# Performance work log

Measured on AMD Instinct MI355X. Metric: run time of the kernel, lower is better.

The kernel has to match this reference:

```python
import jax, jax.numpy as jnp
import numpy as np

# ---- Cl(3,0) Cayley table; blade order [1, e1,e2,e3, e12,e13,e23, e123] ----
def _build_cayley():
    blades = [0b000, 0b001, 0b010, 0b100, 0b011, 0b101, 0b110, 0b111]
    pos = {b: i for i, b in enumerate(blades)}
    def sign(a, b):
        s, a = 0, a >> 1
        while a:
            s += bin(a & b).count('1')
            a >>= 1
        return -1.0 if s & 1 else 1.0
    C = np.zeros((8, 8, 8), np.float32)
    for i, a in enumerate(blades):
        for k, b in enumerate(blades):
            C[i, pos[a ^ b], k] = sign(a, b)  # e_a * e_b -> sign * e_(a^b), metric all +1
    return jnp.asarray(C)

CAYLEY = _build_cayley()
EPS = 1e-6
SEQ = 25      # num_nodes (5) + num_edges (20)
HEADS = 8

def _expand_grades(w):
    # [..., 4] (per-grade) -> [..., 8] (per-blade), grade dims 1,3,3,1
    return jnp.concatenate([w[..., 0:1],
                            jnp.repeat(w[..., 1:2], 3, -1),
                            jnp.repeat(w[..., 2:3], 3, -1),
                            w[..., 3:4]], axis=-1)

def mv_linear(x, w, b):
    # x [N, in, 8], w [out, in, 4], b [out]; bias only on scalar blade
    y = jnp.einsum('nmi,omi->noi', x, _expand_grades(w))
    return y.at[..., 0].add(b)

def mv_layernorm(x, a):
    n = jnp.linalg.norm(x, axis=-1, keepdims=True)   # [N, c, 1] multivector norm
    n = jnp.mean(n, axis=1, keepdims=True) + EPS     # mean over channels -> [N, 1, 1]
    return a[None, :, None] * x / n

def mv_silu(x, a, b):
    # invariants: scalar component + squared grade magnitudes (mag2)
    inv = jnp.stack([x[..., 0],
                     jnp.sum(x[..., 1:4] ** 2, -1),
                     jnp.sum(x[..., 4:7] ** 2, -1),
                     x[..., 7] ** 2], axis=-1)       # [N, c, 4]
    return _expand_grades(jax.nn.sigmoid(a * inv + b)) * x

def geometric_product(a, b):
    return jnp.einsum('nci,ijk,nck->ncj', a, CAYLEY, b)


def setup_inputs() -> dict:
    key = jax.random.key(0)
    ks = iter(jax.random.split(key, 40))
    D, B = 128, 1024
    N = B * SEQ
    s = 0.05
    rn = lambda *sh: jax.random.normal(next(ks), sh, jnp.float32) * s
    return dict(
        src=jax.random.normal(next(ks), (N, D, 8), jnp.float32),
        ln1_a=jnp.ones(D, jnp.float32), ln2_a=jnp.ones(D, jnp.float32), ln3_a=jnp.ones(D, jnp.float32),
        wq=rn(D, D, 4), bq=jnp.zeros(D, jnp.float32),
        wk=rn(D, D, 4), bk=jnp.zeros(D, jnp.float32),
        wv=rn(D, D, 4), bv=jnp.zeros(D, jnp.float32),
        wo=rn(D, D, 4), bo=jnp.zeros(D, jnp.float32),
        gw1=rn(2 * D, D, 4), gb1=jnp.zeros(2 * D, jnp.float32),
        gw2=rn(2 * D, D, 4), gb2=jnp.zeros(2 * D, jnp.float32),
        gw3=rn(D, 2 * D, 4), gb3=jnp.zeros(D, jnp.float32),
        gna=jnp.ones(D, jnp.float32),
        mw1=rn(2 * D, D, 4), mb1=jnp.zeros(2 * D, jnp.float32),
        sa=jnp.ones((2 * D, 4), jnp.float32), sb=jnp.zeros((2 * D, 4), jnp.float32),
        mw2=rn(D, 2 * D, 4), mb2=jnp.zeros(D, jnp.float32),
    )


def reference(src, ln1_a, ln2_a, ln3_a, wq, bq, wk, bk, wv, bv, wo, bo,
              gw1, gb1, gw2, gb2, gw3, gb3, gna,
              mw1, mb1, sa, sb, mw2, mb2):
    N, D, _ = src.shape
    B, dh = N // SEQ, D // HEADS

    def attention(x):
        q = mv_linear(x, wq, bq).reshape(B, SEQ, HEADS, dh, 8)
        k = mv_linear(x, wk, bk).reshape(B, SEQ, HEADS, dh, 8)
        v = mv_linear(x, wv, bv).reshape(B, SEQ, HEADS, dh, 8)
        scores = jnp.einsum('bshdi,bthdi->bhst', q, k) / np.float32(np.sqrt(dh * 8))
        p = jax.nn.softmax(scores, axis=-1)
        o = jnp.einsum('bhst,bthdi->bshdi', p, v).reshape(N, D, 8)
        return mv_linear(o, wo, bo)

    # pre-norm attention + residual
    x = src + attention(mv_layernorm(src, ln1_a))
    x = mv_layernorm(x, ln2_a)
    # GP_Layer: two grade-wise linears -> geometric product -> linear -> norm
    xl = mv_linear(x, gw1, gb1)
    xr = mv_linear(x, gw2, gb2)
    g = mv_layernorm(mv_linear(geometric_product(xl, xr), gw3, gb3), gna)
    x = x + g
    x = mv_layernorm(x, ln3_a)
    # gated MLP: MVLinear -> MVSiLU -> MVLinear
    ff = mv_linear(mv_silu(mv_linear(x, mw1, mb1), sa, sb), mw2, mb2)
    return x + ff
```

## Files before the change

### kernel.cpp

```cpp
#include <hip/hip_runtime.h>
#include <hip/hip_bf16.h>
#include <math.h>

#define NROWS 25600
#define SEQL  25
#define EPSV  1e-6f

typedef __hip_bfloat16 bf16;
typedef __attribute__((ext_vector_type(4))) float f32x4;
typedef __attribute__((ext_vector_type(8))) short bf16x8;
typedef unsigned int u32;

#define GLD16(gp_, lp_) __builtin_amdgcn_global_load_lds( \
    (const __attribute__((address_space(1))) u32*)(gp_), \
    (__attribute__((address_space(3))) u32*)(lp_), 16, 0, 0)

__device__ __forceinline__ void gprod(const float* a, const float* b, float* r) {
  const int M[8] = {0,1,2,4,3,5,6,7};
  const int P[8] = {0,1,2,4,3,5,6,7};
#pragma unroll
  for (int i = 0; i < 8; ++i) {
    const int ma = M[i];
#pragma unroll
    for (int k = 0; k < 8; ++k) {
      const int mb = M[k];
      int par = 0;
      for (int t = ma >> 1; t; t >>= 1) par += __popc(t & mb);
      const float s = (par & 1) ? -1.f : 1.f;
      r[P[ma ^ mb]] += s * a[i] * b[k];
    }
  }
}

template<int KT, int ON>
__global__ __launch_bounds__(256) void gemm_kernel(
    const bf16* __restrict__ A, const bf16* __restrict__ W,
    const float* __restrict__ bias, const float* __restrict__ invnm,
    bf16* __restrict__ Y)
{
  __shared__ __align__(16) short As[128 * 128];
  __shared__ __align__(16) short Bs[128 * 128];
  const int tid  = threadIdx.x;
  const int lane = tid & 63;
  const int wid  = tid >> 6;
  const int pl   = blockIdx.z;
  const int g    = (pl == 0) ? 0 : ((pl < 4) ? 1 : ((pl < 7) ? 2 : 3));
  const size_t n0 = (size_t)blockIdx.x * 128;
  const int c0    = blockIdx.y * 128;
  const bf16* Ab = A + (size_t)pl * NROWS * KT + n0 * KT;
  const bf16* Wb = W + ((size_t)g * ON + c0) * KT;

  f32x4 acc[4][4];
#pragma unroll
  for (int i = 0; i < 4; ++i)
#pragma unroll
    for (int j = 0; j < 4; ++j) acc[i][j] = (f32x4){0.f, 0.f, 0.f, 0.f};

  const int wm = (wid & 1) * 64;
  const int wn = (wid >> 1) * 64;
  const int srow = wid * 32 + (lane >> 4);
  const int scol = (lane & 15) * 8;

  constexpr int NC = KT / 128;
#pragma unroll
  for (int kc = 0; kc < NC; ++kc) {
#pragma unroll
    for (int j = 0; j < 8; ++j) {
      const bf16* ga = Ab + (size_t)(srow + j * 4) * KT + kc * 128 + scol;
      const bf16* gb = Wb + (size_t)(srow + j * 4) * KT + kc * 128 + scol;
      GLD16(ga, &As[wid * 4096 + j * 512]);
      GLD16(gb, &Bs[wid * 4096 + j * 512]);
    }
    __syncthreads();
#pragma unroll
    for (int ks = 0; ks < 4; ++ks) {
      bf16x8 af[4], bg[4];
#pragma unroll
      for (int i = 0; i < 4; ++i) {
        af[i] = *(const bf16x8*)&As[(wm + i * 16 + (lane & 15)) * 128 + ks * 32 + (lane >> 4) * 8];
        bg[i] = *(const bf16x8*)&Bs[(wn + i * 16 + (lane & 15)) * 128 + ks * 32 + (lane >> 4) * 8];
      }
#pragma unroll
      for (int mi = 0; mi < 4; ++mi)
#pragma unroll
        for (int ni = 0; ni < 4; ++ni)
          acc[mi][ni] = __builtin_amdgcn_mfma_f32_16x16x32_bf16(af[mi], bg[ni], acc[mi][ni], 0, 0, 0);
    }
    if (kc + 1 < NC) __syncthreads();
  }

  const int cr = (lane >> 4) * 4;
  const int cc = lane & 15;
  bf16* Yb = Y + (size_t)pl * NROWS * ON;
#pragma unroll
  for (int mi = 0; mi < 4; ++mi) {
#pragma unroll
    for (int j = 0; j < 4; ++j) {
      const size_t n = n0 + wm + mi * 16 + cr + j;
      const float sc = invnm ? invnm[n] : 1.f;
#pragma unroll
      for (int ni = 0; ni < 4; ++ni) {
        const int colg = c0 + wn + ni * 16 + cc;
        float v = acc[mi][ni][j] * sc;
        if (pl == 0) v += bias[colg];
        Yb[n * ON + colg] = __float2bfloat16(v);
      }
    }
  }
}

__global__ __launch_bounds__(256) void wprep_kernel(
    const float* __restrict__ w, const float* __restrict__ lnscale,
    bf16* __restrict__ out, int O, int K)
{
  const int idx = blockIdx.x * 256 + threadIdx.x;
  if (idx >= O * K) return;
  const int k = idx % K;
  const float s = lnscale ? lnscale[k] : 1.f;
  const float4 wv = *(const float4*)(w + (size_t)idx * 4);
  const size_t P = (size_t)O * K;
  out[0 * P + idx] = __float2bfloat16(wv.x * s);
  out[1 * P + idx] = __float2bfloat16(wv.y * s);
  out[2 * P + idx] = __float2bfloat16(wv.z * s);
  out[3 * P + idx] = __float2bfloat16(wv.w * s);
}

__global__ __launch_bounds__(256) void repack_kernel(
    const float* __restrict__ src, bf16* __restrict__ Xp, float* __restrict__ nminv)
{
  __shared__ float red[256];
  const int tid = threadIdx.x;
  const size_t n = (size_t)blockIdx.x * 2 + (tid >> 7);
  const int c = tid & 127;
  const size_t P = (size_t)NROWS * 128;
  const size_t idx = n * 128 + c;
  const float* sp = src + idx * 8;
  float v[8];
  const float4 s0 = *(const float4*)sp;
  const float4 s1 = *(const float4*)(sp + 4);
  v[0]=s0.x; v[1]=s0.y; v[2]=s0.z; v[3]=s0.w;
  v[4]=s1.x; v[5]=s1.y; v[6]=s1.z; v[7]=s1.w;
  float ss = 0.f;
#pragma unroll
  for (int p = 0; p < 8; ++p) {
    Xp[p * P + idx] = __float2bfloat16(v[p]);
    ss += v[p] * v[p];
  }
  red[tid] = sqrtf(ss);
  __syncthreads();
  for (int off = 64; off > 0; off >>= 1) {
    if ((tid & 127) < off) red[tid] += red[tid + off];
    __syncthreads();
  }
  if (c == 0) nminv[n] = 1.f / (red[tid] / 128.f + EPSV);
}

__global__ __launch_bounds__(256) void attn_kernel(
    bf16* __restrict__ Q, const bf16* __restrict__ K, const bf16* __restrict__ V)
{
  __shared__ float Pld[4][32 * 36];
  const int tid  = threadIdx.x;
  const int lane = tid & 63;
  const int wid  = tid >> 6;
  const int job  = blockIdx.x * 4 + wid;
  const int b    = job >> 3;
  const int h    = job & 7;
  const size_t PS = (size_t)NROWS * 128;
  const int rowbase = b * SEQL;
  const int l15 = lane & 15;
  const int lg  = lane >> 4;

  f32x4 acc[2][2];
#pragma unroll
  for (int si = 0; si < 2; ++si)
#pragma unroll
    for (int ti = 0; ti < 2; ++ti) acc[si][ti] = (f32x4){0.f,0.f,0.f,0.f};

#pragma unroll
  for (int ks = 0; ks < 4; ++ks) {
    const int f = ks * 32 + lg * 8;
    const int p = f >> 4, d = f & 15;
    bf16x8 aq[2], bk[2];
#pragma unroll
    for (int si = 0; si < 2; ++si) {
      int s = si * 16 + l15; if (s > 24) s = 24;
      aq[si] = *(const bf16x8*)(Q + (size_t)p * PS + (size_t)(rowbase + s) * 128 + h * 16 + d);
    }
#pragma unroll
    for (int ti = 0; ti < 2; ++ti) {
      int t = ti * 16 + l15; if (t > 24) t = 24;
      bk[ti] = *(const bf16x8*)(K + (size_t)p * PS + (size_t)(rowbase + t) * 128 + h * 16 + d);
    }
#pragma unroll
    for (int si = 0; si < 2; ++si)
#pragma unroll
      for (int ti = 0; ti < 2; ++ti)
        acc[si][ti] = __builtin_amdgcn_mfma_f32_16x16x32_bf16(aq[si], bk[ti], acc[si][ti], 0, 0, 0);
  }

  const float scale = 0.08838834764831845f;
  float pv[2][2][4];
#pragma unroll
  for (int si = 0; si < 2; ++si)
#pragma unroll
    for (int ti = 0; ti < 2; ++ti)
#pragma unroll
      for (int r = 0; r < 4; ++r) {
        float v = acc[si][ti][r] * scale;
        if (ti * 16 + l15 > 24) v = -1e30f;
        pv[si][ti][r] = v;
      }
#pragma unroll
  for (int si = 0; si < 2; ++si)
#pragma unroll
    for (int r = 0; r < 4; ++r) {
      float m = fmaxf(pv[si][0][r], pv[si][1][r]);
#pragma unroll
      for (int off = 1; off < 16; off <<= 1) m = fmaxf(m, __shfl_xor(m, off));
      const float e0 = __expf(pv[si][0][r] - m);
      const float e1 = __expf(pv[si][1][r] - m);
      float sum = e0 + e1;
#pragma unroll
      for (int off = 1; off < 16; off <<= 1) sum += __shfl_xor(sum, off);
      const float inv = 1.f / sum;
      pv[si][0][r] = e0 * inv;
      pv[si][1][r] = e1 * inv;
    }

  float* Pw = &Pld[wid][0];
#pragma unroll
  for (int si = 0; si < 2; ++si)
#pragma unroll
    for (int ti = 0; ti < 2; ++ti)
#pragma unroll
      for (int r = 0; r < 4; ++r)
        Pw[(si * 16 + lg * 4 + r) * 36 + ti * 16 + l15] = pv[si][ti][r];
  __syncthreads();

  const int p2 = lane >> 3;
  const int d2 = (lane & 7) * 2;
  const bf16* vb = V + (size_t)p2 * PS + (size_t)rowbase * 128 + h * 16 + d2;
  float vlo[32], vhi[32];
#pragma unroll
  for (int t = 0; t < SEQL; ++t) {
    const __hip_bfloat162 vv = *(const __hip_bfloat162*)(vb + (size_t)t * 128);
    vlo[t] = __bfloat162float(vv.x);
    vhi[t] = __bfloat162float(vv.y);
  }
#pragma unroll
  for (int t = SEQL; t < 32; ++t) { vlo[t] = 0.f; vhi[t] = 0.f; }

  bf16* ob = Q + (size_t)p2 * PS + (size_t)rowbase * 128 + h * 16 + d2;
  for (int s = 0; s < SEQL; ++s) {
    const float4* pr = reinterpret_cast<const float4*>(&Pld[wid][s * 36]);
    float a0 = 0.f, a1 = 0.f;
#pragma unroll
    for (int t4 = 0; t4 < 8; ++t4) {
      const float4 pq = pr[t4];
      a0 += pq.x * vlo[t4*4+0] + pq.y * vlo[t4*4+1] + pq.z * vlo[t4*4+2] + pq.w * vlo[t4*4+3];
      a1 += pq.x * vhi[t4*4+0] + pq.y * vhi[t4*4+1] + pq.z * vhi[t4*4+2] + pq.w * vhi[t4*4+3];
    }
    __hip_bfloat162 o2;
    o2.x = __float2bfloat16(a0);
    o2.y = __float2bfloat16(a1);
    *(__hip_bfloat162*)(ob + (size_t)s * 128) = o2;
  }
}

__global__ __launch_bounds__(256) void xres_kernel(
    const float* __restrict__ src, const bf16* __restrict__ AO,
    bf16* __restrict__ X, float* __restrict__ nminv)
{
  __shared__ float red[256];
  const int tid = threadIdx.x;
  const size_t n = (size_t)blockIdx.x * 2 + (tid >> 7);
  const int c = tid & 127;
  const size_t P = (size_t)NROWS * 128;
  const size_t idx = n * 128 + c;
  const float* sp = src + idx * 8;
  float v[8];
  const float4 s0 = *(const float4*)sp;
  const float4 s1 = *(const float4*)(sp + 4);
  v[0]=s0.x; v[1]=s0.y; v[2]=s0.z; v[3]=s0.w;
  v[4]=s1.x; v[5]=s1.y; v[6]=s1.z; v[7]=s1.w;
  float ss = 0.f;
#pragma unroll
  for (int p = 0; p < 8; ++p) {
    v[p] += __bfloat162float(AO[p * P + idx]);
    X[p * P + idx] = __float2bfloat16(v[p]);
    ss += v[p] * v[p];
  }
  red[tid] = sqrtf(ss);
  __syncthreads();
  for (int off = 64; off > 0; off >>= 1) {
    if ((tid & 127) < off) red[tid] += red[tid + off];
    __syncthreads();
  }
  if (c == 0) nminv[n] = 1.f / (red[tid] / 128.f + EPSV);
}

__global__ __launch_bounds__(256) void gp_kernel(
    bf16* __restrict__ XL, const bf16* __restrict__ XR)
{
  const size_t idx = (size_t)blockIdx.x * 256 + threadIdx.x;
  const size_t P = (size_t)NROWS * 256;
  float a[8], b[8], r[8] = {0.f,0.f,0.f,0.f,0.f,0.f,0.f,0.f};
#pragma unroll
  for (int p = 0; p < 8; ++p) {
    a[p] = __bfloat162float(XL[p * P + idx]);
    b[p] = __bfloat162float(XR[p * P + idx]);
  }
  gprod(a, b, r);
#pragma unroll
  for (int p = 0; p < 8; ++p) XL[p * P + idx] = __float2bfloat16(r[p]);
}

__global__ __launch_bounds__(256) void combine_kernel(
    bf16* __restrict__ X, const bf16* __restrict__ Gl,
    const float* __restrict__ ln2a, const float* __restrict__ gna,
    const float* __restrict__ nm2inv, float* __restrict__ nm4inv)
{
  __shared__ float red[256];
  const int tid = threadIdx.x;
  const size_t n = (size_t)blockIdx.x * 2 + (tid >> 7);
  const int c = tid & 127;
  const size_t P = (size_t)NROWS * 128;
  const size_t idx = n * 128 + c;

  float gv[8];
  float ssg = 0.f;
#pragma unroll
  for (int p = 0; p < 8; ++p) {
    gv[p] = __bfloat162float(Gl[p * P + idx]);
    ssg += gv[p] * gv[p];
  }
  red[tid] = sqrtf(ssg);
  __syncthreads();
  for (int off = 64; off > 0; off >>= 1) {
    if ((tid & 127) < off) red[tid] += red[tid + off];
    __syncthreads();
  }
  const float invg = 1.f / (red[tid & 128] / 128.f + EPSV);
  __syncthreads();

  const float s2 = ln2a[c] * nm2inv[n];
  const float sg = gna[c] * invg;
  float ss = 0.f;
#pragma unroll
  for (int p = 0; p < 8; ++p) {
    const float v = s2 * __bfloat162float(X[p * P + idx]) + sg * gv[p];
    X[p * P + idx] = __float2bfloat16(v);
    ss += v * v;
  }
  red[tid] = sqrtf(ss);
  __syncthreads();
  for (int off = 64; off > 0; off >>= 1) {
    if ((tid & 127) < off) red[tid] += red[tid + off];
    __syncthreads();
  }
  if (c == 0) nm4inv[n] = 1.f / (red[tid] / 128.f + EPSV);
}

__global__ __launch_bounds__(256) void silu_kernel(
    bf16* __restrict__ H, const float* __restrict__ sa, const float* __restrict__ sb)
{
  const size_t idx = (size_t)blockIdx.x * 256 + threadIdx.x;
  const int c = (int)(idx & 255);
  const size_t P = (size_t)NROWS * 256;
  float v[8];
#pragma unroll
  for (int p = 0; p < 8; ++p) v[p] = __bfloat162float(H[p * P + idx]);
  const float i0 = v[0];
  const float i1 = v[1]*v[1] + v[2]*v[2] + v[3]*v[3];
  const float i2 = v[4]*v[4] + v[5]*v[5] + v[6]*v[6];
  const float i3 = v[7]*v[7];
  const float g0 = 1.f / (1.f + expf(-(sa[c*4+0]*i0 + sb[c*4+0])));
  const float g1 = 1.f / (1.f + expf(-(sa[c*4+1]*i1 + sb[c*4+1])));
  const float g2 = 1.f / (1.f + expf(-(sa[c*4+2]*i2 + sb[c*4+2])));
  const float g3 = 1.f / (1.f + expf(-(sa[c*4+3]*i3 + sb[c*4+3])));
  v[0]*=g0; v[1]*=g1; v[2]*=g1; v[3]*=g1; v[4]*=g2; v[5]*=g2; v[6]*=g2; v[7]*=g3;
#pragma unroll
  for (int p = 0; p < 8; ++p) H[p * P + idx] = __float2bfloat16(v[p]);
}

__global__ __launch_bounds__(256) void final_kernel(
    const bf16* __restrict__ X3, const bf16* __restrict__ FF,
    const float* __restrict__ ln3a, const float* __restrict__ nm4inv,
    float* __restrict__ out)
{
  const size_t idx = (size_t)blockIdx.x * 256 + threadIdx.x;
  const int c = (int)(idx & 127);
  const size_t n = idx >> 7;
  const size_t P = (size_t)NROWS * 128;
  const float s = ln3a[c] * nm4inv[n];
  float o[8];
#pragma unroll
  for (int p = 0; p < 8; ++p)
    o[p] = s * __bfloat162float(X3[p * P + idx]) + __bfloat162float(FF[p * P + idx]);
  float4 lo, hi;
  lo.x=o[0]; lo.y=o[1]; lo.z=o[2]; lo.w=o[3];
  hi.x=o[4]; hi.y=o[5]; hi.z=o[6]; hi.w=o[7];
  *reinterpret_cast<float4*>(out + idx * 8)     = lo;
  *reinterpret_cast<float4*>(out + idx * 8 + 4) = hi;
}

extern "C" void kernel_launch(void* const* d_in, const int* in_sizes, int n_in,
                              void* d_out, int out_size, void* d_ws, size_t ws_size,
                              hipStream_t stream) {
  (void)in_sizes; (void)n_in; (void)out_size; (void)ws_size;
  const float* src   = (const float*)d_in[0];
  const float* ln1_a = (const float*)d_in[1];
  const float* ln2_a = (const float*)d_in[2];
  const float* ln3_a = (const float*)d_in[3];
  const float* wq = (const float*)d_in[4];  const float* bq = (const float*)d_in[5];
  const float* wk = (const float*)d_in[6];  const float* bk = (const float*)d_in[7];
  const float* wv = (const float*)d_in[8];  const float* bv = (const float*)d_in[9];
  const float* wo = (const float*)d_in[10]; const float* bo = (const float*)d_in[11];
  const float* gw1 = (const float*)d_in[12]; const float* gb1 = (const float*)d_in[13];
  const float* gw2 = (const float*)d_in[14]; const float* gb2 = (const float*)d_in[15];
  const float* gw3 = (const float*)d_in[16]; const float* gb3 = (const float*)d_in[17];
  const float* gna = (const float*)d_in[18];
  const float* mw1 = (const float*)d_in[19]; const float* mb1 = (const float*)d_in[20];
  const float* sa  = (const float*)d_in[21]; const float* sb  = (const float*)d_in[22];
  const float* mw2 = (const float*)d_in[23]; const float* mb2 = (const float*)d_in[24];

  const size_t P128 = (size_t)NROWS * 128;
  char* ws = (char*)d_ws;
  bf16* R1 = (bf16*)ws;
  bf16* R2 = (bf16*)(ws + 104857600);
  bf16* WQ = (bf16*)(ws + 157286400);
  bf16* WK = WQ + 65536;
  bf16* WV = WK + 65536;
  bf16* WO = WV + 65536;
  bf16* WG1 = WO + 65536;
  bf16* WG2 = WG1 + 131072;
  bf16* WG3 = WG2 + 131072;
  bf16* WM1 = WG3 + 131072;
  bf16* WM2 = WM1 + 131072;
  float* nm1 = (float*)(ws + 159121408);
  float* nm2 = nm1 + NROWS;
  float* nm4 = nm2 + NROWS;

  bf16* Dd = (bf16*)d_out;
  bf16* Xp = R2;
  bf16* Kp = R1;
  bf16* Vp = R1 + P128;

  wprep_kernel<<<64, 256, 0, stream>>>(wq, ln1_a, WQ, 128, 128);
  wprep_kernel<<<64, 256, 0, stream>>>(wk, ln1_a, WK, 128, 128);
  wprep_kernel<<<64, 256, 0, stream>>>(wv, ln1_a, WV, 128, 128);
  wprep_kernel<<<64, 256, 0, stream>>>(wo, nullptr, WO, 128, 128);
  wprep_kernel<<<128, 256, 0, stream>>>(gw1, ln2_a, WG1, 256, 128);
  wprep_kernel<<<128, 256, 0, stream>>>(gw2, ln2_a, WG2, 256, 128);
  wprep_kernel<<<128, 256, 0, stream>>>(gw3, nullptr, WG3, 128, 256);
  wprep_kernel<<<128, 256, 0, stream>>>(mw1, ln3_a, WM1, 256, 128);
  wprep_kernel<<<128, 256, 0, stream>>>(mw2, nullptr, WM2, 128, 256);

  repack_kernel<<<NROWS / 2, 256, 0, stream>>>(src, Xp, nm1);

  dim3 g128(NROWS / 128, 1, 8), g256(NROWS / 128, 2, 8);
  gemm_kernel<128, 128><<<g128, 256, 0, stream>>>(Xp, WQ, bq, nm1, Dd);
  gemm_kernel<128, 128><<<g128, 256, 0, stream>>>(Xp, WK, bk, nm1, Kp);
  gemm_kernel<128, 128><<<g128, 256, 0, stream>>>(Xp, WV, bv, nm1, Vp);

  attn_kernel<<<2048, 256, 0, stream>>>(Dd, Kp, Vp);

  gemm_kernel<128, 128><<<g128, 256, 0, stream>>>(Dd, WO, bo, nullptr, Kp);

  xres_kernel<<<NROWS / 2, 256, 0, stream>>>(src, Kp, Xp, nm2);

  gemm_kernel<128, 256><<<g256, 256, 0, stream>>>(Xp, WG1, gb1, nm2, Dd);
  gemm_kernel<128, 256><<<g256, 256, 0, stream>>>(Xp, WG2, gb2, nm2, R1);

  gp_kernel<<<NROWS, 256, 0, stream>>>(Dd, R1);

  gemm_kernel<256, 128><<<g128, 256, 0, stream>>>(Dd, WG3, gb3, nullptr, Kp);

  combine_kernel<<<NROWS / 2, 256, 0, stream>>>(Xp, Kp, ln2_a, gna, nm2, nm4);

  gemm_kernel<128, 256><<<g256, 256, 0, stream>>>(Xp, WM1, mb1, nm4, Dd);

  silu_kernel<<<NROWS, 256, 0, stream>>>(Dd, sa, sb);

  gemm_kernel<256, 128><<<g128, 256, 0, stream>>>(Dd, WM2, mb2, nullptr, Vp);

  final_kernel<<<(NROWS * 128) / 256, 256, 0, stream>>>(Xp, Vp, ln3_a, nm4, (float*)d_out);
}
```

Before: 681.2 us.

## Swizzle GEMM LDS layout, vectorize elementwise kernels, merge weight prep launches

The GEMM shared-memory tiles now use an XOR swizzle on the 16-byte column chunk, so fragment reads stop colliding on LDS banks. Each elementwise kernel (repack, xres, gp, combine, silu, final) now handles four channels per thread with 8-byte bf16 vector loads and stores. The shared-memory tree reductions are replaced by wavefront shuffle reductions, and the nine weight-prep launches become one. Silu also switches to the fast __expf, which trades a little accuracy.

```diff
diff --git a/kernel.cpp b/kernel.cpp
--- a/kernel.cpp
+++ b/kernel.cpp
@@ -9,11 +9,20 @@
 typedef __hip_bfloat16 bf16;
 typedef __attribute__((ext_vector_type(4))) float f32x4;
 typedef __attribute__((ext_vector_type(8))) short bf16x8;
+typedef __attribute__((ext_vector_type(4))) short s16x4;
 typedef unsigned int u32;
 
 #define GLD16(gp_, lp_) __builtin_amdgcn_global_load_lds( \
     (const __attribute__((address_space(1))) u32*)(gp_), \
     (__attribute__((address_space(3))) u32*)(lp_), 16, 0, 0)
+
+__device__ __forceinline__ float b2f(short s) {
+  return __uint_as_float(((u32)(unsigned short)s) << 16);
+}
+__device__ __forceinline__ short f2b(float f) {
+  __hip_bfloat16 h = __float2bfloat16(f);
+  return *reinterpret_cast<short*>(&h);
+}
 
 __device__ __forceinline__ void gprod(const float* a, const float* b, float* r) {
   const int M[8] = {0,1,2,4,3,5,6,7};
@@ -58,16 +67,19 @@
 
   const int wm = (wid & 1) * 64;
   const int wn = (wid >> 1) * 64;
-  const int srow = wid * 32 + (lane >> 4);
-  const int scol = (lane & 15) * 8;
+  const int lg  = lane >> 4;
+  const int c8  = lane & 15;
+  const int l15 = lane & 15;
 
   constexpr int NC = KT / 128;
 #pragma unroll
   for (int kc = 0; kc < NC; ++kc) {
 #pragma unroll
     for (int j = 0; j < 8; ++j) {
-      const bf16* ga = Ab + (size_t)(srow + j * 4) * KT + kc * 128 + scol;
-      const bf16* gb = Wb + (size_t)(srow + j * 4) * KT + kc * 128 + scol;
+      const int row = wid * 32 + j * 4 + lg;
+      const int sw = (c8 ^ (row & 7)) * 8;
+      const bf16* ga = Ab + (size_t)row * KT + kc * 128 + sw;
+      const bf16* gb = Wb + (size_t)row * KT + kc * 128 + sw;
       GLD16(ga, &As[wid * 4096 + j * 512]);
       GLD16(gb, &Bs[wid * 4096 + j * 512]);
     }
@@ -77,8 +89,10 @@
       bf16x8 af[4], bg[4];
 #pragma unroll
       for (int i = 0; i < 4; ++i) {
-        af[i] = *(const bf16x8*)&As[(wm + i * 16 + (lane & 15)) * 128 + ks * 32 + (lane >> 4) * 8];
-        bg[i] = *(const bf16x8*)&Bs[(wn + i * 16 + (lane & 15)) * 128 + ks * 32 + (lane >> 4) * 8];
+        const int rA = wm + i * 16 + l15;
+        const int rB = wn + i * 16 + l15;
+        af[i] = *(const bf16x8*)&As[rA * 128 + (((ks * 4 + lg) ^ (rA & 7)) * 8)];
+        bg[i] = *(const bf16x8*)&Bs[rB * 128 + (((ks * 4 + lg) ^ (rB & 7)) * 8)];
       }
 #pragma unroll
       for (int mi = 0; mi < 4; ++mi)
@@ -109,50 +123,63 @@
   }
 }
 
-__global__ __launch_bounds__(256) void wprep_kernel(
-    const float* __restrict__ w, const float* __restrict__ lnscale,
-    bf16* __restrict__ out, int O, int K)
-{
-  const int idx = blockIdx.x * 256 + threadIdx.x;
-  if (idx >= O * K) return;
+__global__ __launch_bounds__(256) void wprep_all_kernel(
+    const float* wq, const float* wk, const float* wv, const float* wo,
+    const float* gw1, const float* gw2, const float* gw3,
+    const float* mw1, const float* mw2,
+    const float* ln1, const float* ln2, const float* ln3,
+    bf16* WQ, bf16* WK, bf16* WV, bf16* WO,
+    bf16* WG1, bf16* WG2, bf16* WG3, bf16* WM1, bf16* WM2)
+{
+  const int gid = blockIdx.x * 256 + threadIdx.x;
+  const float* w; const float* ln; bf16* out; int K; int idx; int sz;
+  if      (gid <  16384) { w=wq;  ln=ln1;     out=WQ;  K=128; idx=gid;          sz=16384; }
+  else if (gid <  32768) { w=wk;  ln=ln1;     out=WK;  K=128; idx=gid-16384;    sz=16384; }
+  else if (gid <  49152) { w=wv;  ln=ln1;     out=WV;  K=128; idx=gid-32768;    sz=16384; }
+  else if (gid <  65536) { w=wo;  ln=nullptr; out=WO;  K=128; idx=gid-49152;    sz=16384; }
+  else if (gid <  98304) { w=gw1; ln=ln2;     out=WG1; K=128; idx=gid-65536;    sz=32768; }
+  else if (gid < 131072) { w=gw2; ln=ln2;     out=WG2; K=128; idx=gid-98304;    sz=32768; }
+  else if (gid < 163840) { w=gw3; ln=nullptr; out=WG3; K=256; idx=gid-131072;   sz=32768; }
+  else if (gid < 196608) { w=mw1; ln=ln3;     out=WM1; K=128; idx=gid-163840;   sz=32768; }
+  else                   { w=mw2; ln=nullptr; out=WM2; K=256; idx=gid-196608;   sz=32768; }
   const int k = idx % K;
-  const float s = lnscale ? lnscale[k] : 1.f;
-  const float4 wv = *(const float4*)(w + (size_t)idx * 4);
-  const size_t P = (size_t)O * K;
-  out[0 * P + idx] = __float2bfloat16(wv.x * s);
-  out[1 * P + idx] = __float2bfloat16(wv.y * s);
-  out[2 * P + idx] = __float2bfloat16(wv.z * s);
-  out[3 * P + idx] = __float2bfloat16(wv.w * s);
+  const float s = ln ? ln[k] : 1.f;
+  const float4 wv4 = *(const float4*)(w + (size_t)idx * 4);
+  out[0 * sz + idx] = __float2bfloat16(wv4.x * s);
+  out[1 * sz + idx] = __float2bfloat16(wv4.y * s);
+  out[2 * sz + idx] = __float2bfloat16(wv4.z * s);
+  out[3 * sz + idx] = __float2bfloat16(wv4.w * s);
 }
 
 __global__ __launch_bounds__(256) void repack_kernel(
     const float* __restrict__ src, bf16* __restrict__ Xp, float* __restrict__ nminv)
 {
-  __shared__ float red[256];
   const int tid = threadIdx.x;
-  const size_t n = (size_t)blockIdx.x * 2 + (tid >> 7);
-  const int c = tid & 127;
+  const size_t base = ((size_t)blockIdx.x * 256 + tid) * 4;
   const size_t P = (size_t)NROWS * 128;
-  const size_t idx = n * 128 + c;
-  const float* sp = src + idx * 8;
-  float v[8];
-  const float4 s0 = *(const float4*)sp;
-  const float4 s1 = *(const float4*)(sp + 4);
-  v[0]=s0.x; v[1]=s0.y; v[2]=s0.z; v[3]=s0.w;
-  v[4]=s1.x; v[5]=s1.y; v[6]=s1.z; v[7]=s1.w;
-  float ss = 0.f;
+  float v[4][8];
+  const float4* sp = (const float4*)(src + base * 8);
+  float part = 0.f;
+#pragma unroll
+  for (int e = 0; e < 4; ++e) {
+    const float4 a = sp[e * 2], b = sp[e * 2 + 1];
+    v[e][0]=a.x; v[e][1]=a.y; v[e][2]=a.z; v[e][3]=a.w;
+    v[e][4]=b.x; v[e][5]=b.y; v[e][6]=b.z; v[e][7]=b.w;
+    float ss = 0.f;
+#pragma unroll
+    for (int p = 0; p < 8; ++p) ss += v[e][p] * v[e][p];
+    part += sqrtf(ss);
+  }
 #pragma unroll
   for (int p = 0; p < 8; ++p) {
-    Xp[p * P + idx] = __float2bfloat16(v[p]);
-    ss += v[p] * v[p];
-  }
-  red[tid] = sqrtf(ss);
-  __syncthreads();
-  for (int off = 64; off > 0; off >>= 1) {
-    if ((tid & 127) < off) red[tid] += red[tid + off];
-    __syncthreads();
-  }
-  if (c == 0) nminv[n] = 1.f / (red[tid] / 128.f + EPSV);
+    s16x4 o;
+#pragma unroll
+    for (int e = 0; e < 4; ++e) o[e] = f2b(v[e][p]);
+    *(s16x4*)(Xp + p * P + base) = o;
+  }
+#pragma unroll
+  for (int off = 1; off < 32; off <<= 1) part += __shfl_xor(part, off);
+  if ((tid & 31) == 0) nminv[base >> 7] = 1.f / (part / 128.f + EPSV);
 }
 
 __global__ __launch_bounds__(256) void attn_kernel(
@@ -271,48 +298,60 @@
     const float* __restrict__ src, const bf16* __restrict__ AO,
     bf16* __restrict__ X, float* __restrict__ nminv)
 {
-  __shared__ float red[256];
   const int tid = threadIdx.x;
-  const size_t n = (size_t)blockIdx.x * 2 + (tid >> 7);
-  const int c = tid & 127;
+  const size_t base = ((size_t)blockIdx.x * 256 + tid) * 4;
   const size_t P = (size_t)NROWS * 128;
-  const size_t idx = n * 128 + c;
-  const float* sp = src + idx * 8;
-  float v[8];
-  const float4 s0 = *(const float4*)sp;
-  const float4 s1 = *(const float4*)(sp + 4);
-  v[0]=s0.x; v[1]=s0.y; v[2]=s0.z; v[3]=s0.w;
-  v[4]=s1.x; v[5]=s1.y; v[6]=s1.z; v[7]=s1.w;
-  float ss = 0.f;
+  float v[4][8];
+  const float4* sp = (const float4*)(src + base * 8);
+#pragma unroll
+  for (int e = 0; e < 4; ++e) {
+    const float4 a = sp[e * 2], b = sp[e * 2 + 1];
+    v[e][0]=a.x; v[e][1]=a.y; v[e][2]=a.z; v[e][3]=a.w;
+    v[e][4]=b.x; v[e][5]=b.y; v[e][6]=b.z; v[e][7]=b.w;
+  }
+  float part = 0.f;
+  float ss[4] = {0.f, 0.f, 0.f, 0.f};
 #pragma unroll
   for (int p = 0; p < 8; ++p) {
-    v[p] += __bfloat162float(AO[p * P + idx]);
-    X[p * P + idx] = __float2bfloat16(v[p]);
-    ss += v[p] * v[p];
-  }
-  red[tid] = sqrtf(ss);
-  __syncthreads();
-  for (int off = 64; off > 0; off >>= 1) {
-    if ((tid & 127) < off) red[tid] += red[tid + off];
-    __syncthreads();
-  }
-  if (c == 0) nminv[n] = 1.f / (red[tid] / 128.f + EPSV);
+    const s16x4 av = *(const s16x4*)(AO + p * P + base);
+    s16x4 o;
+#pragma unroll
+    for (int e = 0; e < 4; ++e) {
+      v[e][p] += b2f(av[e]);
+      o[e] = f2b(v[e][p]);
+      ss[e] += v[e][p] * v[e][p];
+    }
+    *(s16x4*)(X + p * P + base) = o;
+  }
+#pragma unroll
+  for (int e = 0; e < 4; ++e) part += sqrtf(ss[e]);
+#pragma unroll
+  for (int off = 1; off < 32; off <<= 1) part += __shfl_xor(part, off);
+  if ((tid & 31) == 0) nminv[base >> 7] = 1.f / (part / 128.f + EPSV);
 }
 
 __global__ __launch_bounds__(256) void gp_kernel(
     bf16* __restrict__ XL, const bf16* __restrict__ XR)
 {
-  const size_t idx = (size_t)blockIdx.x * 256 + threadIdx.x;
+  const size_t base = ((size_t)blockIdx.x * 256 + threadIdx.x) * 4;
   const size_t P = (size_t)NROWS * 256;
-  float a[8], b[8], r[8] = {0.f,0.f,0.f,0.f,0.f,0.f,0.f,0.f};
+  s16x4 av[8], bv[8], rv[8];
 #pragma unroll
   for (int p = 0; p < 8; ++p) {
-    a[p] = __bfloat162float(XL[p * P + idx]);
-    b[p] = __bfloat162float(XR[p * P + idx]);
-  }
-  gprod(a, b, r);
-#pragma unroll
-  for (int p = 0; p < 8; ++p) XL[p * P + idx] = __float2bfloat16(r[p]);
+    av[p] = *(const s16x4*)(XL + p * P + base);
+    bv[p] = *(const s16x4*)(XR + p * P + base);
+  }
+#pragma unroll
+  for (int e = 0; e < 4; ++e) {
+    float a[8], b[8], r[8] = {0.f,0.f,0.f,0.f,0.f,0.f,0.f,0.f};
+#pragma unroll
+    for (int p = 0; p < 8; ++p) { a[p] = b2f(av[p][e]); b[p] = b2f(bv[p][e]); }
+    gprod(a, b, r);
+#pragma unroll
+    for (int p = 0; p < 8; ++p) rv[p][e] = f2b(r[p]);
+  }
+#pragma unroll
+  for (int p = 0; p < 8; ++p) *(s16x4*)(XL + p * P + base) = rv[p];
 }
 
 __global__ __launch_bounds__(256) void combine_kernel(
@@ -320,67 +359,78 @@
     const float* __restrict__ ln2a, const float* __restrict__ gna,
     const float* __restrict__ nm2inv, float* __restrict__ nm4inv)
 {
-  __shared__ float red[256];
   const int tid = threadIdx.x;
-  const size_t n = (size_t)blockIdx.x * 2 + (tid >> 7);
-  const int c = tid & 127;
+  const size_t base = ((size_t)blockIdx.x * 256 + tid) * 4;
   const size_t P = (size_t)NROWS * 128;
-  const size_t idx = n * 128 + c;
-
-  float gv[8];
-  float ssg = 0.f;
+  const size_t n = base >> 7;
+  const int c = (int)(base & 127);
+
+  float gv[4][8];
+  float ssg[4] = {0.f,0.f,0.f,0.f};
 #pragma unroll
   for (int p = 0; p < 8; ++p) {
-    gv[p] = __bfloat162float(Gl[p * P + idx]);
-    ssg += gv[p] * gv[p];
-  }
-  red[tid] = sqrtf(ssg);
-  __syncthreads();
-  for (int off = 64; off > 0; off >>= 1) {
-    if ((tid & 127) < off) red[tid] += red[tid + off];
-    __syncthreads();
-  }
-  const float invg = 1.f / (red[tid & 128] / 128.f + EPSV);
-  __syncthreads();
-
-  const float s2 = ln2a[c] * nm2inv[n];
-  const float sg = gna[c] * invg;
-  float ss = 0.f;
+    const s16x4 g4 = *(const s16x4*)(Gl + p * P + base);
+#pragma unroll
+    for (int e = 0; e < 4; ++e) { gv[e][p] = b2f(g4[e]); ssg[e] += gv[e][p] * gv[e][p]; }
+  }
+  float partg = sqrtf(ssg[0]) + sqrtf(ssg[1]) + sqrtf(ssg[2]) + sqrtf(ssg[3]);
+#pragma unroll
+  for (int off = 1; off < 32; off <<= 1) partg += __shfl_xor(partg, off);
+  const float invg = 1.f / (partg / 128.f + EPSV);
+
+  const float n2 = nm2inv[n];
+  float s2[4], sg[4];
+#pragma unroll
+  for (int e = 0; e < 4; ++e) { s2[e] = ln2a[c + e] * n2; sg[e] = gna[c + e] * invg; }
+
+  float ss[4] = {0.f,0.f,0.f,0.f};
 #pragma unroll
   for (int p = 0; p < 8; ++p) {
-    const float v = s2 * __bfloat162float(X[p * P + idx]) + sg * gv[p];
-    X[p * P + idx] = __float2bfloat16(v);
-    ss += v * v;
-  }
-  red[tid] = sqrtf(ss);
-  __syncthreads();
-  for (int off = 64; off > 0; off >>= 1) {
-    if ((tid & 127) < off) red[tid] += red[tid + off];
-    __syncthreads();
-  }
-  if (c == 0) nm4inv[n] = 1.f / (red[tid] / 128.f + EPSV);
+    const s16x4 x4 = *(const s16x4*)(X + p * P + base);
+    s16x4 o;
+#pragma unroll
+    for (int e = 0; e < 4; ++e) {
+      const float v = s2[e] * b2f(x4[e]) + sg[e] * gv[e][p];
+      o[e] = f2b(v);
+      ss[e] += v * v;
+    }
+    *(s16x4*)(X + p * P + base) = o;
+  }
+  float part = sqrtf(ss[0]) + sqrtf(ss[1]) + sqrtf(ss[2]) + sqrtf(ss[3]);
+#pragma unroll
+  for (int off = 1; off < 32; off <<= 1) part += __shfl_xor(part, off);
+  if ((tid & 31) == 0) nm4inv[n] = 1.f / (part / 128.f + EPSV);
 }
 
 __global__ __launch_bounds__(256) void silu_kernel(
     bf16* __restrict__ H, const float* __restrict__ sa, const float* __restrict__ sb)
 {
-  const size_t idx = (size_t)blockIdx.x * 256 + threadIdx.x;
-  const int c = (int)(idx & 255);
+  const size_t base = ((size_t)blockIdx.x * 256 + threadIdx.x) * 4;
+  const int c = (int)(base & 255);
   const size_t P = (size_t)NROWS * 256;
-  float v[8];
-#pragma unroll
-  for (int p = 0; p < 8; ++p) v[p] = __bfloat162float(H[p * P + idx]);
-  const float i0 = v[0];
-  const float i1 = v[1]*v[1] + v[2]*v[2] + v[3]*v[3];
-  const float i2 = v[4]*v[4] + v[5]*v[5] + v[6]*v[6];
-  const float i3 = v[7]*v[7];
-  const float g0 = 1.f / (1.f + expf(-(sa[c*4+0]*i0 + sb[c*4+0])));
-  const float g1 = 1.f / (1.f + expf(-(sa[c*4+1]*i1 + sb[c*4+1])));
-  const float g2 = 1.f / (1.f + expf(-(sa[c*4+2]*i2 + sb[c*4+2])));
-  const float g3 = 1.f / (1.f + expf(-(sa[c*4+3]*i3 + sb[c*4+3])));
-  v[0]*=g0; v[1]*=g1; v[2]*=g1; v[3]*=g1; v[4]*=g2; v[5]*=g2; v[6]*=g2; v[7]*=g3;
-#pragma unroll
-  for (int p = 0; p < 8; ++p) H[p * P + idx] = __float2bfloat16(v[p]);
+  s16x4 hv[8];
+#pragma unroll
+  for (int p = 0; p < 8; ++p) hv[p] = *(const s16x4*)(H + p * P + base);
+#pragma unroll
+  for (int e = 0; e < 4; ++e) {
+    float v[8];
+#pragma unroll
+    for (int p = 0; p < 8; ++p) v[p] = b2f(hv[p][e]);
+    const float i0 = v[0];
+    const float i1 = v[1]*v[1] + v[2]*v[2] + v[3]*v[3];
+    const float i2 = v[4]*v[4] + v[5]*v[5] + v[6]*v[6];
+    const float i3 = v[7]*v[7];
+    const int cc = c + e;
+    const float g0 = 1.f / (1.f + __expf(-(sa[cc*4+0]*i0 + sb[cc*4+0])));
+    const float g1 = 1.f / (1.f + __expf(-(sa[cc*4+1]*i1 + sb[cc*4+1])));
+    const float g2 = 1.f / (1.f + __expf(-(sa[cc*4+2]*i2 + sb[cc*4+2])));
+    const float g3 = 1.f / (1.f + __expf(-(sa[cc*4+3]*i3 + sb[cc*4+3])));
+    v[0]*=g0; v[1]*=g1; v[2]*=g1; v[3]*=g1; v[4]*=g2; v[5]*=g2; v[6]*=g2; v[7]*=g3;
+#pragma unroll
+    for (int p = 0; p < 8; ++p) hv[p][e] = f2b(v[p]);
+  }
+#pragma unroll
+  for (int p = 0; p < 8; ++p) *(s16x4*)(H + p * P + base) = hv[p];
 }
 
 __global__ __launch_bounds__(256) void final_kernel(
@@ -388,20 +438,29 @@
     const float* __restrict__ ln3a, const float* __restrict__ nm4inv,
     float* __restrict__ out)
 {
-  const size_t idx = (size_t)blockIdx.x * 256 + threadIdx.x;
-  const int c = (int)(idx & 127);
-  const size_t n = idx >> 7;
+  const size_t base = ((size_t)blockIdx.x * 256 + threadIdx.x) * 4;
+  const int c = (int)(base & 127);
+  const size_t n = base >> 7;
   const size_t P = (size_t)NROWS * 128;
-  const float s = ln3a[c] * nm4inv[n];
-  float o[8];
-#pragma unroll
-  for (int p = 0; p < 8; ++p)
-    o[p] = s * __bfloat162float(X3[p * P + idx]) + __bfloat162float(FF[p * P + idx]);
-  float4 lo, hi;
-  lo.x=o[0]; lo.y=o[1]; lo.z=o[2]; lo.w=o[3];
-  hi.x=o[4]; hi.y=o[5]; hi.z=o[6]; hi.w=o[7];
-  *reinterpret_cast<float4*>(out + idx * 8)     = lo;
-  *reinterpret_cast<float4*>(out + idx * 8 + 4) = hi;
+  const float nm = nm4inv[n];
+  float o[4][8];
+#pragma unroll
+  for (int p = 0; p < 8; ++p) {
+    const s16x4 x4 = *(const s16x4*)(X3 + p * P + base);
+    const s16x4 f4 = *(const s16x4*)(FF + p * P + base);
+#pragma unroll
+    for (int e = 0; e < 4; ++e)
+      o[e][p] = ln3a[c + e] * nm * b2f(x4[e]) + b2f(f4[e]);
+  }
+  float4* op = (float4*)(out + base * 8);
+#pragma unroll
+  for (int e = 0; e < 4; ++e) {
+    float4 lo, hi;
+    lo.x=o[e][0]; lo.y=o[e][1]; lo.z=o[e][2]; lo.w=o[e][3];
+    hi.x=o[e][4]; hi.y=o[e][5]; hi.z=o[e][6]; hi.w=o[e][7];
+    op[e * 2] = lo;
+    op[e * 2 + 1] = hi;
+  }
 }
 
 extern "C" void kernel_launch(void* const* d_in, const int* in_sizes, int n_in,
@@ -446,17 +505,12 @@
   bf16* Kp = R1;
   bf16* Vp = R1 + P128;
 
-  wprep_kernel<<<64, 256, 0, stream>>>(wq, ln1_a, WQ, 128, 128);
-  wprep_kernel<<<64, 256, 0, stream>>>(wk, ln1_a, WK, 128, 128);
-  wprep_kernel<<<64, 256, 0, stream>>>(wv, ln1_a, WV, 128, 128);
-  wprep_kernel<<<64, 256, 0, stream>>>(wo, nullptr, WO, 128, 128);
-  wprep_kernel<<<128, 256, 0, stream>>>(gw1, ln2_a, WG1, 256, 128);
-  wprep_kernel<<<128, 256, 0, stream>>>(gw2, ln2_a, WG2, 256, 128);
-  wprep_kernel<<<128, 256, 0, stream>>>(gw3, nullptr, WG3, 128, 256);
-  wprep_kernel<<<128, 256, 0, stream>>>(mw1, ln3_a, WM1, 256, 128);
-  wprep_kernel<<<128, 256, 0, stream>>>(mw2, nullptr, WM2, 128, 256);
-
-  repack_kernel<<<NROWS / 2, 256, 0, stream>>>(src, Xp, nm1);
+  wprep_all_kernel<<<896, 256, 0, stream>>>(
+      wq, wk, wv, wo, gw1, gw2, gw3, mw1, mw2,
+      ln1_a, ln2_a, ln3_a,
+      WQ, WK, WV, WO, WG1, WG2, WG3, WM1, WM2);
+
+  repack_kernel<<<3200, 256, 0, stream>>>(src, Xp, nm1);
 
   dim3 g128(NROWS / 128, 1, 8), g256(NROWS / 128, 2, 8);
   gemm_kernel<128, 128><<<g128, 256, 0, stream>>>(Xp, WQ, bq, nm1, Dd);
@@ -467,22 +521,22 @@
 
   gemm_kernel<128, 128><<<g128, 256, 0, stream>>>(Dd, WO, bo, nullptr, Kp);
 
-  xres_kernel<<<NROWS / 2, 256, 0, stream>>>(src, Kp, Xp, nm2);
+  xres_kernel<<<3200, 256, 0, stream>>>(src, Kp, Xp, nm2);
 
   gemm_kernel<128, 256><<<g256, 256, 0, stream>>>(Xp, WG1, gb1, nm2, Dd);
   gemm_kernel<128, 256><<<g256, 256, 0, stream>>>(Xp, WG2, gb2, nm2, R1);
 
-  gp_kernel<<<NROWS, 256, 0, stream>>>(Dd, R1);
+  gp_kernel<<<6400, 256, 0, stream>>>(Dd, R1);
 
   gemm_kernel<256, 128><<<g128, 256, 0, stream>>>(Dd, WG3, gb3, nullptr, Kp);
 
-  combine_kernel<<<NROWS / 2, 256, 0, stream>>>(Xp, Kp, ln2_a, gna, nm2, nm4);
+  combine_kernel<<<3200, 256, 0, stream>>>(Xp, Kp, ln2_a, gna, nm2, nm4);
 
   gemm_kernel<128, 256><<<g256, 256, 0, stream>>>(Xp, WM1, mb1, nm4, Dd);
 
-  silu_kernel<<<NROWS, 256, 0, stream>>>(Dd, sa, sb);
+  silu_kernel<<<6400, 256, 0, stream>>>(Dd, sa, sb);
 
   gemm_kernel<256, 128><<<g128, 256, 0, stream>>>(Dd, WM2, mb2, nullptr, Vp);
 
-  final_kernel<<<(NROWS * 128) / 256, 256, 0, stream>>>(Xp, Vp, ln3_a, nm4, (float*)d_out);
-}
+  final_kernel<<<3200, 256, 0, stream>>>(Xp, Vp, ln3_a, nm4, (float*)d_out);
+}
```

Result: faster. 620.6 us (-8.9%).
